# Kernel tuning notes

Hardware: AMD Instinct MI355X
Metric: run time of the kernel (lower is better)

## Reference

```python
import jax, jax.numpy as jnp
import numpy as np

N_USERS = 50000
N_ITEMS = 50000
E = 400000
S = 128   # in_feats_s (memory / GRU hidden)
T = 64    # in_feats_t (time encoding dim)
ED = 64   # edge feature dim
M = 2 * S + T + ED  # in_feats_m = 384

_BASIS_FREQ = jnp.asarray(1.0 / 10 ** np.linspace(0, 9, T), dtype=jnp.float32)


def time_encode(ts):
    # cos(ts * freq + phase), phase == 0
    return jnp.cos(ts[:, None] * _BASIS_FREQ[None, :])


def mean_message(src_mem, dst_mem, ts, e, src, dst, n_dst):
    # mail per edge: [E, 2S + T + ED]
    mail = jnp.concatenate(
        [src_mem[src], dst_mem[dst], time_encode(ts), e], axis=1)
    s = jax.ops.segment_sum(mail, dst, num_segments=n_dst)
    cnt = jax.ops.segment_sum(jnp.ones_like(ts), dst, num_segments=n_dst)
    return s / jnp.maximum(cnt, 1.0)[:, None]


def gru_step(x, h, w_ih, w_hh, b_ih, b_hh):
    # single-step PyTorch GRU; gate order r, z, n
    gi = x @ w_ih.T + b_ih
    gh = h @ w_hh.T + b_hh
    ir, iz, i_n = jnp.split(gi, 3, axis=1)
    hr, hz, h_n = jnp.split(gh, 3, axis=1)
    r = jax.nn.sigmoid(ir + hr)
    z = jax.nn.sigmoid(iz + hz)
    n = jnp.tanh(i_n + r * h_n)
    return (1.0 - z) * n + z * h


def setup_inputs() -> dict:
    key = jax.random.key(0)
    ks = jax.random.split(key, 16)
    sc = 1.0 / np.sqrt(S)
    return {
        "si":   jax.random.normal(ks[0], (N_USERS, S), jnp.float32),
        "sj":   jax.random.normal(ks[1], (N_ITEMS, S), jnp.float32),
        "si_r": jax.random.normal(ks[2], (N_ITEMS, S), jnp.float32),
        "sj_r": jax.random.normal(ks[3], (N_USERS, S), jnp.float32),
        "t":    jax.random.uniform(ks[4], (E,), jnp.float32),
        "t_r":  jax.random.uniform(ks[5], (E,), jnp.float32),
        "e":    jax.random.normal(ks[6], (E, ED), jnp.float32),
        "e_r":  jax.random.normal(ks[7], (E, ED), jnp.float32),
        "w_ih": jax.random.normal(ks[8], (3 * S, M), jnp.float32) * sc,
        "w_hh": jax.random.normal(ks[9], (3 * S, S), jnp.float32) * sc,
        "b_ih": jax.random.normal(ks[10], (3 * S,), jnp.float32) * sc,
        "b_hh": jax.random.normal(ks[11], (3 * S,), jnp.float32) * sc,
        "src_g":  jax.random.randint(ks[12], (E,), 0, N_USERS, jnp.int32),
        "dst_g":  jax.random.randint(ks[13], (E,), 0, N_ITEMS, jnp.int32),
        "src_gr": jax.random.randint(ks[14], (E,), 0, N_ITEMS, jnp.int32),
        "dst_gr": jax.random.randint(ks[15], (E,), 0, N_USERS, jnp.int32),
    }


def reference(si, sj, si_r, sj_r, t, t_r, e, e_r,
              w_ih, w_hh, b_ih, b_hh,
              src_g, dst_g, src_gr, dst_gr):
    # g: user -> item; g_r: item -> user
    mj = mean_message(si, sj, t, e, src_g, dst_g, N_ITEMS)       # messages to items
    mi = mean_message(si_r, sj_r, t_r, e_r, src_gr, dst_gr, N_USERS)  # messages to users
    si_out = gru_step(mi, sj_r, w_ih, w_hh, b_ih, b_hh)  # user memory update
    sj_out = gru_step(mj, sj, w_ih, w_hh, b_ih, b_hh)    # item memory update
    return (si_out, sj_out)
```

## Files before the change

kernel.cpp:

```cpp
#include <hip/hip_runtime.h>
#include <math.h>

#define NUSERS 50000
#define NITEMS 50000
#define NTOT   100000
#define NNODE  50000
#define NCHUNK 196
#define MTILES 6250
#define KDIM   512

typedef __attribute__((ext_vector_type(4))) float f32x4;
typedef __attribute__((ext_vector_type(8))) short short8;
typedef unsigned int u32;

#define AS1 __attribute__((address_space(1)))
#define AS3 __attribute__((address_space(3)))

static __device__ __forceinline__ unsigned short f2bf(float f) {
  unsigned int u = __float_as_uint(f);
  u += 0x7fffu + ((u >> 16) & 1u);
  return (unsigned short)(u >> 16);
}

static __device__ __forceinline__ u32 pack2(float x, float y) {
  return (u32)f2bf(x) | ((u32)f2bf(y) << 16);
}

static __device__ __forceinline__ void gload_lds16(const void* g, void* l) {
  __builtin_amdgcn_global_load_lds((const AS1 u32*)g, (AS3 u32*)l, 16, 0, 0);
}

__global__ void pack_w_kernel(const float* __restrict__ w_ih,
                              const float* __restrict__ w_hh,
                              const float* __restrict__ b_ih,
                              const float* __restrict__ b_hh,
                              unsigned short* __restrict__ Wb,
                              float* __restrict__ bb) {
  int idx = blockIdx.x * 256 + threadIdx.x;
  int j = idx & 7, l = (idx >> 3) & 63, ktt = idx >> 9;
  int kt = ktt & 15, tt = ktt >> 4;
  int g = tt * 16 + (l & 15);
  int k = kt * 32 + (l >> 4) * 8 + j;
  float v;
  if (g < 256)      v = (k < 384) ? w_ih[g * 384 + k] : w_hh[g * 128 + (k - 384)];
  else if (g < 384) v = (k < 384) ? w_ih[g * 384 + k] : 0.0f;
  else              v = (k < 384) ? 0.0f : w_hh[(g - 128) * 128 + (k - 384)];
  Wb[idx] = f2bf(v);
  if (idx < 512) {
    float b = (idx < 256) ? (b_ih[idx] + b_hh[idx])
            : (idx < 384) ? b_ih[idx]
                          : b_hh[idx - 128];
    bb[idx] = b;
  }
}

__global__ void cast_mem_kernel(const float* __restrict__ si,
                                const float* __restrict__ si_r,
                                unsigned short* __restrict__ si_b,
                                unsigned short* __restrict__ sir_b) {
  int i = blockIdx.x * 256 + threadIdx.x;
  const float* src; unsigned short* dst; int off;
  if (i < 800000) { src = si;   dst = si_b;  off = i; }
  else            { src = si_r; dst = sir_b; off = i - 800000; }
  const f32x4* p = (const f32x4*)(src + (size_t)off * 8);
  f32x4 a = p[0], b = p[1];
  short8 o;
  o[0] = f2bf(a[0]); o[1] = f2bf(a[1]); o[2] = f2bf(a[2]); o[3] = f2bf(a[3]);
  o[4] = f2bf(b[0]); o[5] = f2bf(b[1]); o[6] = f2bf(b[2]); o[7] = f2bf(b[3]);
  *(short8*)(dst + (size_t)off * 8) = o;
}

__global__ void hist_kernel(const int* __restrict__ dst_g,
                            const int* __restrict__ dst_gr,
                            int* __restrict__ deg_j, int* __restrict__ deg_i, int E) {
  int i = blockIdx.x * 256 + threadIdx.x;
  if (i < E) atomicAdd(&deg_j[dst_g[i]], 1);
  else if (i < 2 * E) atomicAdd(&deg_i[dst_gr[i - E]], 1);
}

__global__ void chunksum_kernel(const int* __restrict__ deg_j,
                                const int* __restrict__ deg_i,
                                int* __restrict__ csum) {
  int c = blockIdx.x;
  const int* deg = (c < NCHUNK) ? deg_j : deg_i;
  int cc = (c < NCHUNK) ? c : c - NCHUNK;
  int t = threadIdx.x;
  int idx = cc * 256 + t;
  int v = (idx < NNODE) ? deg[idx] : 0;
  for (int off = 32; off; off >>= 1) v += __shfl_down(v, off, 64);
  __shared__ int wsum[4];
  if ((t & 63) == 0) wsum[t >> 6] = v;
  __syncthreads();
  if (t == 0) csum[c] = wsum[0] + wsum[1] + wsum[2] + wsum[3];
}

__global__ void chunkscan_kernel(const int* __restrict__ csum, int* __restrict__ coff) {
  int d = blockIdx.x;
  const int* cs = csum + d * NCHUNK;
  int* co = coff + d * NCHUNK;
  int t = threadIdx.x, lane = t & 63, w = t >> 6;
  int v = (t < NCHUNK) ? cs[t] : 0;
  int x = v;
  for (int off = 1; off < 64; off <<= 1) {
    int y = __shfl_up(x, off, 64);
    if (lane >= off) x += y;
  }
  __shared__ int wt[4];
  if (lane == 63) wt[w] = x;
  __syncthreads();
  int add = 0;
  for (int k = 0; k < 4; ++k) if (k < w) add += wt[k];
  if (t < NCHUNK) co[t] = add + x - v;
}

__global__ void localscan_kernel(const int* __restrict__ deg_j,
                                 const int* __restrict__ deg_i,
                                 const int* __restrict__ coff,
                                 int* __restrict__ rs_j, int* __restrict__ cur_j,
                                 int* __restrict__ rs_i, int* __restrict__ cur_i) {
  int c = blockIdx.x;
  bool dj = c < NCHUNK;
  const int* deg = dj ? deg_j : deg_i;
  int cc = dj ? c : c - NCHUNK;
  int* rs = dj ? rs_j : rs_i;
  int* cur = dj ? cur_j : cur_i;
  int base = coff[c];
  int t = threadIdx.x, lane = t & 63, w = t >> 6;
  int idx = cc * 256 + t;
  int v = (idx < NNODE) ? deg[idx] : 0;
  int x = v;
  for (int off = 1; off < 64; off <<= 1) {
    int y = __shfl_up(x, off, 64);
    if (lane >= off) x += y;
  }
  __shared__ int wt[4];
  if (lane == 63) wt[w] = x;
  __syncthreads();
  int add = 0;
  for (int k = 0; k < 4; ++k) if (k < w) add += wt[k];
  int ex = base + add + x - v;
  if (idx < NNODE) { rs[idx] = ex; cur[idx] = ex; }
}

__global__ void fill_kernel(const int* __restrict__ src_g, const int* __restrict__ dst_g,
                            const float* __restrict__ t,
                            const int* __restrict__ src_gr, const int* __restrict__ dst_gr,
                            const float* __restrict__ t_r,
                            int* __restrict__ cur_j, int* __restrict__ cur_i,
                            int4* __restrict__ recP_j, int4* __restrict__ recP_i,
                            int E) {
  int i = blockIdx.x * 256 + threadIdx.x;
  if (i < E) {
    int pos = atomicAdd(&cur_j[dst_g[i]], 1);
    recP_j[pos] = make_int4(src_g[i], i, __float_as_int(t[i]), 0);
  } else if (i < 2 * E) {
    int k = i - E;
    int pos = atomicAdd(&cur_i[dst_gr[k]], 1);
    recP_i[pos] = make_int4(src_gr[k], k, __float_as_int(t_r[k]), 0);
  }
}

__global__ __launch_bounds__(256) void gather_kernel(
    const unsigned short* __restrict__ si_b, const unsigned short* __restrict__ sir_b,
    const float* __restrict__ sj, const float* __restrict__ sj_r,
    const float* __restrict__ e, const float* __restrict__ e_r,
    const int* __restrict__ rs_j, const int* __restrict__ rs_i,
    const int* __restrict__ deg_j, const int* __restrict__ deg_i,
    const int4* __restrict__ recP_j, const int4* __restrict__ recP_i,
    unsigned short* __restrict__ Xb) {
  __shared__ __align__(16) unsigned short rowbuf[4][512];
  int wid = threadIdx.x >> 6, lane = threadIdx.x & 63;
  int node = blockIdx.x * 4 + wid;
  bool user = node < NUSERS;
  int idx = user ? node : node - NUSERS;
  const unsigned short* smem = user ? sir_b : si_b;
  const float* h    = user ? sj_r : sj;
  const float* ef   = user ? e_r : e;
  int start = __builtin_amdgcn_readfirstlane((user ? rs_i : rs_j)[idx]);
  int deg   = __builtin_amdgcn_readfirstlane((user ? deg_i : deg_j)[idx]);
  const int4* rec = user ? recP_i : recP_j;

  float freq = __expf((float)lane * -0.3289407276f);
  float2 hvf = *(const float2*)(h + (size_t)idx * 128 + 2 * lane);

  float asx = 0.f, asy = 0.f;
  float at  = 0.f;
  float ae  = 0.f;

  for (int base = 0; base < deg; base += 64) {
    int nn = deg - base; if (nn > 64) nn = 64;
    int cl = (lane < nn) ? base + lane : base + nn - 1;
    int4 r = rec[start + cl];
    for (int j0 = 0; j0 < nn; j0 += 8) {
      int j1 = (j0 + 1 < nn) ? j0 + 1 : nn - 1;
      int j2 = (j0 + 2 < nn) ? j0 + 2 : nn - 1;
      int j3 = (j0 + 3 < nn) ? j0 + 3 : nn - 1;
      int j4 = (j0 + 4 < nn) ? j0 + 4 : nn - 1;
      int j5 = (j0 + 5 < nn) ? j0 + 5 : nn - 1;
      int j6 = (j0 + 6 < nn) ? j0 + 6 : nn - 1;
      int j7 = (j0 + 7 < nn) ? j0 + 7 : nn - 1;
      float w1 = (j0 + 1 < nn) ? 1.0f : 0.0f;
      float w2 = (j0 + 2 < nn) ? 1.0f : 0.0f;
      float w3 = (j0 + 3 < nn) ? 1.0f : 0.0f;
      float w4 = (j0 + 4 < nn) ? 1.0f : 0.0f;
      float w5 = (j0 + 5 < nn) ? 1.0f : 0.0f;
      float w6 = (j0 + 6 < nn) ? 1.0f : 0.0f;
      float w7 = (j0 + 7 < nn) ? 1.0f : 0.0f;

      int s0 = __builtin_amdgcn_readlane(r.x, j0), e0 = __builtin_amdgcn_readlane(r.y, j0);
      int s1 = __builtin_amdgcn_readlane(r.x, j1), e1 = __builtin_amdgcn_readlane(r.y, j1);
      int s2 = __builtin_amdgcn_readlane(r.x, j2), e2 = __builtin_amdgcn_readlane(r.y, j2);
      int s3 = __builtin_amdgcn_readlane(r.x, j3), e3 = __builtin_amdgcn_readlane(r.y, j3);
      int s4 = __builtin_amdgcn_readlane(r.x, j4), e4 = __builtin_amdgcn_readlane(r.y, j4);
      int s5 = __builtin_amdgcn_readlane(r.x, j5), e5 = __builtin_amdgcn_readlane(r.y, j5);
      int s6 = __builtin_amdgcn_readlane(r.x, j6), e6 = __builtin_amdgcn_readlane(r.y, j6);
      int s7 = __builtin_amdgcn_readlane(r.x, j7), e7 = __builtin_amdgcn_readlane(r.y, j7);

      u32 v0 = *(const u32*)(smem + ((size_t)s0 << 7) + 2 * lane);
      u32 v1 = *(const u32*)(smem + ((size_t)s1 << 7) + 2 * lane);
      u32 v2 = *(const u32*)(smem + ((size_t)s2 << 7) + 2 * lane);
      u32 v3 = *(const u32*)(smem + ((size_t)s3 << 7) + 2 * lane);
      u32 v4 = *(const u32*)(smem + ((size_t)s4 << 7) + 2 * lane);
      u32 v5 = *(const u32*)(smem + ((size_t)s5 << 7) + 2 * lane);
      u32 v6 = *(const u32*)(smem + ((size_t)s6 << 7) + 2 * lane);
      u32 v7 = *(const u32*)(smem + ((size_t)s7 << 7) + 2 * lane);
      float f0 = ef[((size_t)e0 << 6) + lane];
      float f1 = ef[((size_t)e1 << 6) + lane];
      float f2 = ef[((size_t)e2 << 6) + lane];
      float f3 = ef[((size_t)e3 << 6) + lane];
      float f4 = ef[((size_t)e4 << 6) + lane];
      float f5 = ef[((size_t)e5 << 6) + lane];
      float f6 = ef[((size_t)e6 << 6) + lane];
      float f7 = ef[((size_t)e7 << 6) + lane];

      float c0 = __cosf(__int_as_float(__builtin_amdgcn_readlane(r.z, j0)) * freq);
      float c1 = __cosf(__int_as_float(__builtin_amdgcn_readlane(r.z, j1)) * freq);
      float c2 = __cosf(__int_as_float(__builtin_amdgcn_readlane(r.z, j2)) * freq);
      float c3 = __cosf(__int_as_float(__builtin_amdgcn_readlane(r.z, j3)) * freq);
      float c4 = __cosf(__int_as_float(__builtin_amdgcn_readlane(r.z, j4)) * freq);
      float c5 = __cosf(__int_as_float(__builtin_amdgcn_readlane(r.z, j5)) * freq);
      float c6 = __cosf(__int_as_float(__builtin_amdgcn_readlane(r.z, j6)) * freq);
      float c7 = __cosf(__int_as_float(__builtin_amdgcn_readlane(r.z, j7)) * freq);

      float l0 = __uint_as_float(v0 << 16), g0 = __uint_as_float(v0 & 0xffff0000u);
      float l1 = __uint_as_float(v1 << 16), g1 = __uint_as_float(v1 & 0xffff0000u);
      float l2 = __uint_as_float(v2 << 16), g2 = __uint_as_float(v2 & 0xffff0000u);
      float l3 = __uint_as_float(v3 << 16), g3 = __uint_as_float(v3 & 0xffff0000u);
      float l4 = __uint_as_float(v4 << 16), g4 = __uint_as_float(v4 & 0xffff0000u);
      float l5 = __uint_as_float(v5 << 16), g5 = __uint_as_float(v5 & 0xffff0000u);
      float l6 = __uint_as_float(v6 << 16), g6 = __uint_as_float(v6 & 0xffff0000u);
      float l7 = __uint_as_float(v7 << 16), g7 = __uint_as_float(v7 & 0xffff0000u);

      asx += l0 + w1 * l1 + w2 * l2 + w3 * l3 + w4 * l4 + w5 * l5 + w6 * l6 + w7 * l7;
      asy += g0 + w1 * g1 + w2 * g2 + w3 * g3 + w4 * g4 + w5 * g5 + w6 * g6 + w7 * g7;
      at  += c0 + w1 * c1 + w2 * c2 + w3 * c3 + w4 * c4 + w5 * c5 + w6 * c6 + w7 * c7;
      ae  += f0 + w1 * f1 + w2 * f2 + w3 * f3 + w4 * f4 + w5 * f5 + w6 * f6 + w7 * f7;
    }
  }

  float invc = (deg > 0) ? 1.0f / (float)deg : 0.0f;
  float hz   = (deg > 0) ? 1.0f : 0.0f;

  unsigned short* rb = rowbuf[wid];
  u32* rb32 = (u32*)rb;
  rb32[lane]       = pack2(asx * invc, asy * invc);
  rb32[64 + lane]  = pack2(hvf.x * hz, hvf.y * hz);
  rb[256 + lane]   = f2bf(at * invc);
  rb[320 + lane]   = f2bf(ae * invc);
  rb32[192 + lane] = pack2(hvf.x, hvf.y);

  int rt = node >> 4, m = node & 15;
  int kt2 = lane >> 2, q2 = lane & 3;
  short8 vv = *(const short8*)(rb + lane * 8);
  *(short8*)(Xb + (((size_t)rt * 16 + kt2) * 64 + q2 * 16 + m) * 8) = vv;
}

__global__ __launch_bounds__(512, 2) void gemm_gru_kernel(
    const unsigned short* __restrict__ Xb,
    const unsigned short* __restrict__ Wb,
    const float* __restrict__ bb,
    const float* __restrict__ sj_r,
    const float* __restrict__ sj,
    float* __restrict__ out) {
  __shared__ __align__(16) unsigned short sB[2][32768];
  int wid = threadIdx.x >> 6, lane = threadIdx.x & 63;
  int mbase = blockIdx.x * 4;
  int col16 = lane & 15, quad = lane >> 4;

  f32x4 acc[4][4];
#pragma unroll
  for (int mi = 0; mi < 4; ++mi)
#pragma unroll
    for (int g = 0; g < 4; ++g) acc[mi][g] = (f32x4)0.0f;

#define STAGE(buf, s)                                                        \
  {                                                                          \
    _Pragma("unroll")                                                        \
    for (int i = 0; i < 8; ++i) {                                            \
      int c = wid * 8 + i;                                                   \
      int tt = c >> 1, kt = (s) * 2 + (c & 1);                               \
      const unsigned short* gp = Wb + ((size_t)(tt * 16 + kt) * 64 + lane) * 8; \
      gload_lds16(gp, sB[buf] + c * 512);                                    \
    }                                                                        \
  }

  STAGE(0, 0)
  __syncthreads();

  for (int s = 0; s < 8; ++s) {
    int cur = s & 1;
    if (s < 7) STAGE(cur ^ 1, s + 1)
    short8 bfr[4][2];
#pragma unroll
    for (int g = 0; g < 4; ++g)
#pragma unroll
      for (int kp = 0; kp < 2; ++kp) {
        int c = (g * 8 + wid) * 2 + kp;
        bfr[g][kp] = *(const short8*)(sB[cur] + c * 512 + lane * 8);
      }
#pragma unroll
    for (int mi = 0; mi < 4; ++mi) {
      int mt = mbase + mi;
      if (mt >= MTILES) mt = 0;
      const unsigned short* Ab = Xb + (size_t)mt * 8192;
      short8 a0 = *(const short8*)(Ab + (size_t)(s * 2) * 512 + lane * 8);
      short8 a1 = *(const short8*)(Ab + (size_t)(s * 2 + 1) * 512 + lane * 8);
#pragma unroll
      for (int g = 0; g < 4; ++g) {
        acc[mi][g] = __builtin_amdgcn_mfma_f32_16x16x32_bf16(a0, bfr[g][0], acc[mi][g], 0, 0, 0);
        acc[mi][g] = __builtin_amdgcn_mfma_f32_16x16x32_bf16(a1, bfr[g][1], acc[mi][g], 0, 0, 0);
      }
    }
    __syncthreads();
  }

  int c = wid * 16 + col16;
  float bbr = bb[c], bbz = bb[128 + c], bbn = bb[256 + c], bbh = bb[384 + c];
#pragma unroll
  for (int mi = 0; mi < 4; ++mi) {
    int mt = mbase + mi;
    if (mt >= MTILES) continue;
#pragma unroll
    for (int r = 0; r < 4; ++r) {
      int row = mt * 16 + quad * 4 + r;
      float rp  = acc[mi][0][r] + bbr;
      float zp  = acc[mi][1][r] + bbz;
      float inp = acc[mi][2][r] + bbn;
      float hnp = acc[mi][3][r] + bbh;
      float rg = 1.0f / (1.0f + __expf(-rp));
      float zg = 1.0f / (1.0f + __expf(-zp));
      float ng = tanhf(inp + rg * hnp);
      float hv = (row < NUSERS) ? sj_r[(size_t)row * 128 + c]
                                : sj[(size_t)(row - NUSERS) * 128 + c];
      out[(size_t)row * 128 + c] = (1.0f - zg) * ng + zg * hv;
    }
  }
}

extern "C" void kernel_launch(void* const* d_in, const int* in_sizes, int n_in,
                              void* d_out, int out_size, void* d_ws, size_t ws_size,
                              hipStream_t stream) {
  const float* si   = (const float*)d_in[0];
  const float* sj   = (const float*)d_in[1];
  const float* si_r = (const float*)d_in[2];
  const float* sj_r = (const float*)d_in[3];
  const float* t    = (const float*)d_in[4];
  const float* t_r  = (const float*)d_in[5];
  const float* e    = (const float*)d_in[6];
  const float* e_r  = (const float*)d_in[7];
  const float* w_ih = (const float*)d_in[8];
  const float* w_hh = (const float*)d_in[9];
  const float* b_ih = (const float*)d_in[10];
  const float* b_hh = (const float*)d_in[11];
  const int* src_g  = (const int*)d_in[12];
  const int* dst_g  = (const int*)d_in[13];
  const int* src_gr = (const int*)d_in[14];
  const int* dst_gr = (const int*)d_in[15];
  int E = in_sizes[4];

  unsigned short* Xb = (unsigned short*)d_ws;
  unsigned short* Wb = Xb + (size_t)MTILES * 8192;
  float* bb   = (float*)(Wb + 262144);
  int* deg_j  = (int*)(bb + 512);
  int* deg_i  = deg_j + NNODE;
  int* rs_j   = deg_i + NNODE;
  int* rs_i   = rs_j + NNODE;
  int* cur_j  = rs_i + NNODE;
  int* cur_i  = cur_j + NNODE;
  int* csum   = cur_i + NNODE;
  int* coff   = csum + 2 * NCHUNK;
  int4* recP_j = (int4*)(coff + 2 * NCHUNK);
  int4* recP_i = recP_j + E;
  unsigned short* si_b  = (unsigned short*)(recP_i + E);
  unsigned short* sir_b = si_b + 6400000;

  hipMemsetAsync(deg_j, 0, 2 * NNODE * sizeof(int), stream);

  pack_w_kernel<<<(512 * 512) / 256, 256, 0, stream>>>(w_ih, w_hh, b_ih, b_hh, Wb, bb);
  cast_mem_kernel<<<6250, 256, 0, stream>>>(si, si_r, si_b, sir_b);

  int blks2E = (2 * E + 255) / 256;
  hist_kernel<<<blks2E, 256, 0, stream>>>(dst_g, dst_gr, deg_j, deg_i, E);
  chunksum_kernel<<<2 * NCHUNK, 256, 0, stream>>>(deg_j, deg_i, csum);
  chunkscan_kernel<<<2, 256, 0, stream>>>(csum, coff);
  localscan_kernel<<<2 * NCHUNK, 256, 0, stream>>>(deg_j, deg_i, coff, rs_j, cur_j, rs_i, cur_i);
  fill_kernel<<<blks2E, 256, 0, stream>>>(src_g, dst_g, t, src_gr, dst_gr, t_r,
                                          cur_j, cur_i, recP_j, recP_i, E);

  gather_kernel<<<NTOT / 4, 256, 0, stream>>>(si_b, sir_b, sj, sj_r, e, e_r,
                                              rs_j, rs_i, deg_j, deg_i,
                                              recP_j, recP_i, Xb);

  float* out = (float*)d_out;
  gemm_gru_kernel<<<(MTILES + 3) / 4, 512, 0, stream>>>(Xb, Wb, bb, sj_r, sj, out);
}
```

Before: 677.2 us.

## Retile GRU GEMM to 8 M-tiles per block with single-buffered W staging

The GEMM block now covers 8 row tiles instead of 4. Its 8 waves are split into 2 row groups by 4 column groups, and each wave computes 4 row tiles by 8 column subtiles. This halves how many times each W k-slice is loaded into LDS per row tile and cuts shared memory from 128KB to 64KB, so launch bounds rise to allow more blocks per CU. The cost is that the double-buffer prefetch is gone: W loads are issued and awaited each stage with two barriers, and the per-wave accumulator footprint doubles, which adds register pressure.

```diff
diff --git a/kernel.cpp b/kernel.cpp
--- a/kernel.cpp
+++ b/kernel.cpp
@@ -275,84 +275,93 @@
   *(short8*)(Xb + (((size_t)rt * 16 + kt2) * 64 + q2 * 16 + m) * 8) = vv;
 }
 
-__global__ __launch_bounds__(512, 2) void gemm_gru_kernel(
+__global__ __launch_bounds__(512, 4) void gemm_gru_kernel(
     const unsigned short* __restrict__ Xb,
     const unsigned short* __restrict__ Wb,
     const float* __restrict__ bb,
     const float* __restrict__ sj_r,
     const float* __restrict__ sj,
     float* __restrict__ out) {
-  __shared__ __align__(16) unsigned short sB[2][32768];
+  __shared__ __align__(16) unsigned short sB[32768];
   int wid = threadIdx.x >> 6, lane = threadIdx.x & 63;
-  int mbase = blockIdx.x * 4;
+  int mg = wid >> 2, cg = wid & 3;
+  int mbase = blockIdx.x * 8 + mg * 4;
   int col16 = lane & 15, quad = lane >> 4;
 
-  f32x4 acc[4][4];
+  f32x4 acc[4][4][2];
 #pragma unroll
   for (int mi = 0; mi < 4; ++mi)
 #pragma unroll
-    for (int g = 0; g < 4; ++g) acc[mi][g] = (f32x4)0.0f;
-
-#define STAGE(buf, s)                                                        \
-  {                                                                          \
-    _Pragma("unroll")                                                        \
-    for (int i = 0; i < 8; ++i) {                                            \
-      int c = wid * 8 + i;                                                   \
-      int tt = c >> 1, kt = (s) * 2 + (c & 1);                               \
-      const unsigned short* gp = Wb + ((size_t)(tt * 16 + kt) * 64 + lane) * 8; \
-      gload_lds16(gp, sB[buf] + c * 512);                                    \
-    }                                                                        \
-  }
-
-  STAGE(0, 0)
-  __syncthreads();
+    for (int g = 0; g < 4; ++g)
+#pragma unroll
+      for (int nt = 0; nt < 2; ++nt) acc[mi][g][nt] = (f32x4)0.0f;
+
+  const unsigned short* Ap[4];
+#pragma unroll
+  for (int mi = 0; mi < 4; ++mi) {
+    int mt = mbase + mi; if (mt >= MTILES) mt = 0;
+    Ap[mi] = Xb + (size_t)mt * 8192 + lane * 8;
+  }
+  const unsigned short* Wp = Wb + (size_t)(wid * 4) * 16 * 512 + lane * 8;
 
   for (int s = 0; s < 8; ++s) {
-    int cur = s & 1;
-    if (s < 7) STAGE(cur ^ 1, s + 1)
-    short8 bfr[4][2];
+#pragma unroll
+    for (int i = 0; i < 8; ++i) {
+      int tti = i & 3, ktl = i >> 2;
+      const unsigned short* gp = Wp + (size_t)(tti * 16 + s * 2 + ktl) * 512;
+      gload_lds16(gp, sB + (ktl * 32 + wid * 4 + tti) * 512);
+    }
+    short8 a[4][2];
+#pragma unroll
+    for (int mi = 0; mi < 4; ++mi)
+#pragma unroll
+      for (int kp = 0; kp < 2; ++kp)
+        a[mi][kp] = *(const short8*)(Ap[mi] + (size_t)(s * 2 + kp) * 512);
+    __syncthreads();
+    short8 b[4][2][2];
 #pragma unroll
     for (int g = 0; g < 4; ++g)
 #pragma unroll
-      for (int kp = 0; kp < 2; ++kp) {
-        int c = (g * 8 + wid) * 2 + kp;
-        bfr[g][kp] = *(const short8*)(sB[cur] + c * 512 + lane * 8);
+      for (int nt = 0; nt < 2; ++nt) {
+        int tt = g * 8 + cg * 2 + nt;
+#pragma unroll
+        for (int kp = 0; kp < 2; ++kp)
+          b[g][nt][kp] = *(const short8*)(sB + (kp * 32 + tt) * 512 + lane * 8);
       }
+#pragma unroll
+    for (int mi = 0; mi < 4; ++mi)
+#pragma unroll
+      for (int g = 0; g < 4; ++g)
+#pragma unroll
+        for (int nt = 0; nt < 2; ++nt) {
+          acc[mi][g][nt] = __builtin_amdgcn_mfma_f32_16x16x32_bf16(a[mi][0], b[g][nt][0], acc[mi][g][nt], 0, 0, 0);
+          acc[mi][g][nt] = __builtin_amdgcn_mfma_f32_16x16x32_bf16(a[mi][1], b[g][nt][1], acc[mi][g][nt], 0, 0, 0);
+        }
+    __syncthreads();
+  }
+
+#pragma unroll
+  for (int nt = 0; nt < 2; ++nt) {
+    int cc = cg * 32 + nt * 16 + col16;
+    float bbr = bb[cc], bbz = bb[128 + cc], bbn = bb[256 + cc], bbh = bb[384 + cc];
 #pragma unroll
     for (int mi = 0; mi < 4; ++mi) {
       int mt = mbase + mi;
-      if (mt >= MTILES) mt = 0;
-      const unsigned short* Ab = Xb + (size_t)mt * 8192;
-      short8 a0 = *(const short8*)(Ab + (size_t)(s * 2) * 512 + lane * 8);
-      short8 a1 = *(const short8*)(Ab + (size_t)(s * 2 + 1) * 512 + lane * 8);
-#pragma unroll
-      for (int g = 0; g < 4; ++g) {
-        acc[mi][g] = __builtin_amdgcn_mfma_f32_16x16x32_bf16(a0, bfr[g][0], acc[mi][g], 0, 0, 0);
-        acc[mi][g] = __builtin_amdgcn_mfma_f32_16x16x32_bf16(a1, bfr[g][1], acc[mi][g], 0, 0, 0);
+      if (mt >= MTILES) continue;
+#pragma unroll
+      for (int r = 0; r < 4; ++r) {
+        int row = mt * 16 + quad * 4 + r;
+        float rp  = acc[mi][0][nt][r] + bbr;
+        float zp  = acc[mi][1][nt][r] + bbz;
+        float inp = acc[mi][2][nt][r] + bbn;
+        float hnp = acc[mi][3][nt][r] + bbh;
+        float rg = 1.0f / (1.0f + __expf(-rp));
+        float zg = 1.0f / (1.0f + __expf(-zp));
+        float ng = tanhf(inp + rg * hnp);
+        float hv = (row < NUSERS) ? sj_r[(size_t)row * 128 + cc]
+                                  : sj[(size_t)(row - NUSERS) * 128 + cc];
+        out[(size_t)row * 128 + cc] = (1.0f - zg) * ng + zg * hv;
       }
-    }
-    __syncthreads();
-  }
-
-  int c = wid * 16 + col16;
-  float bbr = bb[c], bbz = bb[128 + c], bbn = bb[256 + c], bbh = bb[384 + c];
-#pragma unroll
-  for (int mi = 0; mi < 4; ++mi) {
-    int mt = mbase + mi;
-    if (mt >= MTILES) continue;
-#pragma unroll
-    for (int r = 0; r < 4; ++r) {
-      int row = mt * 16 + quad * 4 + r;
-      float rp  = acc[mi][0][r] + bbr;
-      float zp  = acc[mi][1][r] + bbz;
-      float inp = acc[mi][2][r] + bbn;
-      float hnp = acc[mi][3][r] + bbh;
-      float rg = 1.0f / (1.0f + __expf(-rp));
-      float zg = 1.0f / (1.0f + __expf(-zp));
-      float ng = tanhf(inp + rg * hnp);
-      float hv = (row < NUSERS) ? sj_r[(size_t)row * 128 + c]
-                                : sj[(size_t)(row - NUSERS) * 128 + c];
-      out[(size_t)row * 128 + c] = (1.0f - zg) * ng + zg * hv;
     }
   }
 }
@@ -412,5 +421,5 @@
                                               recP_j, recP_i, Xb);
 
   float* out = (float*)d_out;
-  gemm_gru_kernel<<<(MTILES + 3) / 4, 512, 0, stream>>>(Xb, Wb, bb, sj_r, sj, out);
-}
+  gemm_gru_kernel<<<(MTILES + 7) / 8, 512, 0, stream>>>(Xb, Wb, bb, sj_r, sj, out);
+}
```

After: 1.271 ms. 1.88x slower.

## Restructure GEMM-GRU kernel: stage A tile in LDS, 16 waves split rows and columns

Applied to the files above, without the earlier changes.

The GEMM+GRU kernel now loads the block's whole 64x512 A tile into LDS once, and streams the weight matrix one K-tile at a time through a smaller double buffer. It runs 1024 threads, split into 2 row groups by 8 column groups, instead of 512 threads with each wave covering all 4 M tiles. This removes the repeated direct global reads of A in the inner loop and shrinks each wave's accumulator state, which should raise occupancy. In exchange it needs 16 K-steps, each ending in a barrier across 16 waves. The launch_bounds(1024,4) request may also limit registers per thread.

```diff
diff --git a/kernel.cpp b/kernel.cpp
--- a/kernel.cpp
+++ b/kernel.cpp
@@ -275,70 +275,76 @@
   *(short8*)(Xb + (((size_t)rt * 16 + kt2) * 64 + q2 * 16 + m) * 8) = vv;
 }
 
-__global__ __launch_bounds__(512, 2) void gemm_gru_kernel(
+__global__ __launch_bounds__(1024, 4) void gemm_gru_kernel(
     const unsigned short* __restrict__ Xb,
     const unsigned short* __restrict__ Wb,
     const float* __restrict__ bb,
     const float* __restrict__ sj_r,
     const float* __restrict__ sj,
     float* __restrict__ out) {
-  __shared__ __align__(16) unsigned short sB[2][32768];
+  __shared__ __align__(16) unsigned short sA[32768];
+  __shared__ __align__(16) unsigned short sW[2][16384];
   int wid = threadIdx.x >> 6, lane = threadIdx.x & 63;
+  int mg = wid >> 3, cg = wid & 7;
   int mbase = blockIdx.x * 4;
   int col16 = lane & 15, quad = lane >> 4;
 
-  f32x4 acc[4][4];
-#pragma unroll
-  for (int mi = 0; mi < 4; ++mi)
+  f32x4 acc[2][4];
+#pragma unroll
+  for (int mi = 0; mi < 2; ++mi)
 #pragma unroll
     for (int g = 0; g < 4; ++g) acc[mi][g] = (f32x4)0.0f;
 
-#define STAGE(buf, s)                                                        \
-  {                                                                          \
-    _Pragma("unroll")                                                        \
-    for (int i = 0; i < 8; ++i) {                                            \
-      int c = wid * 8 + i;                                                   \
-      int tt = c >> 1, kt = (s) * 2 + (c & 1);                               \
-      const unsigned short* gp = Wb + ((size_t)(tt * 16 + kt) * 64 + lane) * 8; \
-      gload_lds16(gp, sB[buf] + c * 512);                                    \
-    }                                                                        \
-  }
-
-  STAGE(0, 0)
+#pragma unroll
+  for (int i = 0; i < 4; ++i) {
+    int u = wid * 4 + i;
+    int mt = mbase + (u >> 4);
+    if (mt >= MTILES) mt = MTILES - 1;
+    const unsigned short* gp = Xb + (size_t)mt * 8192 + (u & 15) * 512 + lane * 8;
+    gload_lds16(gp, sA + u * 512);
+  }
+#pragma unroll
+  for (int i = 0; i < 2; ++i) {
+    int tt = wid * 2 + i;
+    const unsigned short* gp = Wb + ((size_t)(tt * 16 + 0) * 64 + lane) * 8;
+    gload_lds16(gp, sW[0] + tt * 512);
+  }
   __syncthreads();
 
-  for (int s = 0; s < 8; ++s) {
-    int cur = s & 1;
-    if (s < 7) STAGE(cur ^ 1, s + 1)
-    short8 bfr[4][2];
-#pragma unroll
-    for (int g = 0; g < 4; ++g)
-#pragma unroll
-      for (int kp = 0; kp < 2; ++kp) {
-        int c = (g * 8 + wid) * 2 + kp;
-        bfr[g][kp] = *(const short8*)(sB[cur] + c * 512 + lane * 8);
-      }
-#pragma unroll
-    for (int mi = 0; mi < 4; ++mi) {
-      int mt = mbase + mi;
-      if (mt >= MTILES) mt = 0;
-      const unsigned short* Ab = Xb + (size_t)mt * 8192;
-      short8 a0 = *(const short8*)(Ab + (size_t)(s * 2) * 512 + lane * 8);
-      short8 a1 = *(const short8*)(Ab + (size_t)(s * 2 + 1) * 512 + lane * 8);
-#pragma unroll
-      for (int g = 0; g < 4; ++g) {
-        acc[mi][g] = __builtin_amdgcn_mfma_f32_16x16x32_bf16(a0, bfr[g][0], acc[mi][g], 0, 0, 0);
-        acc[mi][g] = __builtin_amdgcn_mfma_f32_16x16x32_bf16(a1, bfr[g][1], acc[mi][g], 0, 0, 0);
+  const unsigned short* aBase = sA + (size_t)(mg * 32) * 512 + lane * 8;
+
+  for (int kt = 0; kt < 16; ++kt) {
+    int cur = kt & 1;
+    if (kt < 15) {
+#pragma unroll
+      for (int i = 0; i < 2; ++i) {
+        int tt = wid * 2 + i;
+        const unsigned short* gp = Wb + ((size_t)(tt * 16 + kt + 1) * 64 + lane) * 8;
+        gload_lds16(gp, sW[cur ^ 1] + tt * 512);
       }
     }
+    short8 a0 = *(const short8*)(aBase + (size_t)kt * 512);
+    short8 a1 = *(const short8*)(aBase + (size_t)(16 + kt) * 512);
+    short8 b0 = *(const short8*)(sW[cur] + (0 * 8 + cg) * 512 + lane * 8);
+    short8 b1 = *(const short8*)(sW[cur] + (1 * 8 + cg) * 512 + lane * 8);
+    short8 b2 = *(const short8*)(sW[cur] + (2 * 8 + cg) * 512 + lane * 8);
+    short8 b3 = *(const short8*)(sW[cur] + (3 * 8 + cg) * 512 + lane * 8);
+    acc[0][0] = __builtin_amdgcn_mfma_f32_16x16x32_bf16(a0, b0, acc[0][0], 0, 0, 0);
+    acc[0][1] = __builtin_amdgcn_mfma_f32_16x16x32_bf16(a0, b1, acc[0][1], 0, 0, 0);
+    acc[0][2] = __builtin_amdgcn_mfma_f32_16x16x32_bf16(a0, b2, acc[0][2], 0, 0, 0);
+    acc[0][3] = __builtin_amdgcn_mfma_f32_16x16x32_bf16(a0, b3, acc[0][3], 0, 0, 0);
+    acc[1][0] = __builtin_amdgcn_mfma_f32_16x16x32_bf16(a1, b0, acc[1][0], 0, 0, 0);
+    acc[1][1] = __builtin_amdgcn_mfma_f32_16x16x32_bf16(a1, b1, acc[1][1], 0, 0, 0);
+    acc[1][2] = __builtin_amdgcn_mfma_f32_16x16x32_bf16(a1, b2, acc[1][2], 0, 0, 0);
+    acc[1][3] = __builtin_amdgcn_mfma_f32_16x16x32_bf16(a1, b3, acc[1][3], 0, 0, 0);
     __syncthreads();
   }
 
-  int c = wid * 16 + col16;
-  float bbr = bb[c], bbz = bb[128 + c], bbn = bb[256 + c], bbh = bb[384 + c];
-#pragma unroll
-  for (int mi = 0; mi < 4; ++mi) {
-    int mt = mbase + mi;
+  int cc = cg * 16 + col16;
+  float bbr = bb[cc], bbz = bb[128 + cc], bbn = bb[256 + cc], bbh = bb[384 + cc];
+#pragma unroll
+  for (int mi = 0; mi < 2; ++mi) {
+    int mt = mbase + mg * 2 + mi;
     if (mt >= MTILES) continue;
 #pragma unroll
     for (int r = 0; r < 4; ++r) {
@@ -350,9 +356,9 @@
       float rg = 1.0f / (1.0f + __expf(-rp));
       float zg = 1.0f / (1.0f + __expf(-zp));
       float ng = tanhf(inp + rg * hnp);
-      float hv = (row < NUSERS) ? sj_r[(size_t)row * 128 + c]
-                                : sj[(size_t)(row - NUSERS) * 128 + c];
-      out[(size_t)row * 128 + c] = (1.0f - zg) * ng + zg * hv;
+      float hv = (row < NUSERS) ? sj_r[(size_t)row * 128 + cc]
+                                : sj[(size_t)(row - NUSERS) * 128 + cc];
+      out[(size_t)row * 128 + cc] = (1.0f - zg) * ng + zg * hv;
     }
   }
 }
@@ -412,5 +418,5 @@
                                               recP_j, recP_i, Xb);
 
   float* out = (float*)d_out;
-  gemm_gru_kernel<<<(MTILES + 3) / 4, 512, 0, stream>>>(Xb, Wb, bb, sj_r, sj, out);
-}
+  gemm_gru_kernel<<<(MTILES + 3) / 4, 1024, 0, stream>>>(Xb, Wb, bb, sj_r, sj, out);
+}
```

New measurement: 622.3 us. -8.1%, faster.
